# Kernel optimization log

Hardware: AMD Instinct MI355X
Metric: run time of the kernel (lower is better)

## Reference

```python
import jax, jax.numpy as jnp
import numpy as np

B, S, D, H = 4, 2048, 1024, 16
DEPTH = D // H
NEG = -1e9


def setup_inputs() -> dict:
    key = jax.random.key(0)
    ks = jax.random.split(key, 9)
    scale = 1.0 / np.sqrt(D)
    x = jax.random.normal(ks[0], (B, S, D), dtype=jnp.float32)
    # causal additive mask: 1 where future positions (masked), 0 elsewhere
    mask = jnp.triu(jnp.ones((S, S), dtype=jnp.float32), k=1)[None, None, :, :]
    wq = jax.random.normal(ks[1], (D, D), dtype=jnp.float32) * scale
    bq = jnp.zeros((D,), dtype=jnp.float32)
    wk = jax.random.normal(ks[2], (D, D), dtype=jnp.float32) * scale
    bk = jnp.zeros((D,), dtype=jnp.float32)
    wv = jax.random.normal(ks[3], (D, D), dtype=jnp.float32) * scale
    bv = jnp.zeros((D,), dtype=jnp.float32)
    wo = jax.random.normal(ks[4], (D, D), dtype=jnp.float32) * scale
    bo = jnp.zeros((D,), dtype=jnp.float32)
    return {"x": x, "mask": mask, "wq": wq, "bq": bq, "wk": wk, "bk": bk,
            "wv": wv, "bv": bv, "wo": wo, "bo": bo}


def _split_heads(t):
    # [B, S, D] -> [B, H, S, depth]
    return t.reshape(B, S, H, DEPTH).transpose(0, 2, 1, 3)


def reference(x, mask, wq, bq, wk, bk, wv, bv, wo, bo):
    q = _split_heads(x @ wq.T + bq)
    k = _split_heads(x @ wk.T + bk)
    v = _split_heads(x @ wv.T + bv)
    scores = jnp.einsum('bhqd,bhkd->bhqk', q, k) / jnp.sqrt(jnp.float32(DEPTH))
    scores = scores + mask * NEG
    attn = jax.nn.softmax(scores, axis=-1)
    out = jnp.einsum('bhqk,bhkd->bhqd', attn, v)  # [B, H, S, depth]
    out = out.transpose(0, 2, 1, 3).reshape(B, S, D)
    return out @ wo.T + bo
```

## Files before the change

### kernel.cpp

```cpp
#include <hip/hip_runtime.h>
#include <hip/hip_bf16.h>
#include <stdint.h>

typedef __attribute__((ext_vector_type(8))) short short8;
typedef __attribute__((ext_vector_type(4))) float f32x4;
typedef __attribute__((ext_vector_type(16))) float f32x16;

#define AS1 __attribute__((address_space(1)))
#define AS3 __attribute__((address_space(3)))

constexpr int Bc = 4, Sc = 2048, Dc = 1024, Hc = 16;

__device__ __forceinline__ unsigned short f2b(float x) {
  __hip_bfloat16 h = __float2bfloat16(x);
  return *reinterpret_cast<unsigned short*>(&h);
}

__device__ __forceinline__ uint32_t cvtpk(float lo, float hi) {
  uint32_t r;
  asm("v_cvt_pk_bf16_f32 %0, %1, %2" : "=v"(r) : "v"(lo), "v"(hi));
  return r;
}

__device__ __forceinline__ void glds16(const void* g, void* l) {
  __builtin_amdgcn_global_load_lds((const AS1 uint32_t*)g, (AS3 uint32_t*)l, 16, 0, 0);
}

__global__ void cast_f32_bf16_x4(const float* __restrict__ in,
                                 unsigned short* __restrict__ out, int n4) {
  int i = blockIdx.x * blockDim.x + threadIdx.x;
  if (i >= n4) return;
  float4 a = ((const float4*)in)[i];
  ushort4 o;
  o.x = f2b(a.x); o.y = f2b(a.y); o.z = f2b(a.z); o.w = f2b(a.w);
  ((ushort4*)out)[i] = o;
}

__global__ void cast_w4(const float* __restrict__ wq, const float* __restrict__ wk,
                        const float* __restrict__ wv, const float* __restrict__ wo,
                        unsigned short* __restrict__ oq, unsigned short* __restrict__ ok,
                        unsigned short* __restrict__ ov, unsigned short* __restrict__ oo) {
  int which = blockIdx.y;
  const float* in = which == 0 ? wq : which == 1 ? wk : which == 2 ? wv : wo;
  unsigned short* out = which == 0 ? oq : which == 1 ? ok : which == 2 ? ov : oo;
  int i = blockIdx.x * blockDim.x + threadIdx.x;
  float4 a = ((const float4*)in)[i];
  ushort4 o;
  o.x = f2b(a.x); o.y = f2b(a.y); o.z = f2b(a.z); o.w = f2b(a.w);
  ((ushort4*)out)[i] = o;
}

template<int MODE>
__device__ __forceinline__ void gemm128(
    const unsigned short* __restrict__ A, const unsigned short* __restrict__ W,
    const float* __restrict__ bias, void* __restrict__ outp,
    int m0, int n0, unsigned short (*lA)[128 * 32], unsigned short (*lB)[128 * 32])
{
  const int tid = threadIdx.x;
  const int w = tid >> 6, lane = tid & 63;
  const int g = lane >> 4, c = lane & 15;
  const int wr = w >> 1, wc = w & 1;

  f32x4 acc[4][4];
#pragma unroll
  for (int i = 0; i < 4; ++i)
#pragma unroll
    for (int j = 0; j < 4; ++j) acc[i][j] = f32x4{0.f, 0.f, 0.f, 0.f};

  const int srow = lane >> 2;
  const int gch = (lane & 3) ^ ((srow >> 1) & 3);
  const int rslot = (g ^ ((c >> 1) & 3)) * 16;

  auto stage = [&](int buf, int k0) {
#pragma unroll
    for (int i = 0; i < 2; ++i) {
      int row = i * 64 + w * 16 + srow;
      glds16(A + (size_t)(m0 + row) * 1024 + k0 + gch * 8,
             (char*)lA[buf] + i * 4096 + w * 1024);
      glds16(W + (size_t)(n0 + row) * 1024 + k0 + gch * 8,
             (char*)lB[buf] + i * 4096 + w * 1024);
    }
  };

  stage(0, 0);

  for (int t = 0; t < 32; ++t) {
    const int cur = t & 1;
    if (t + 1 < 32) {
      stage(cur ^ 1, (t + 1) * 32);
      asm volatile("s_waitcnt vmcnt(4)" ::: "memory");
    } else {
      asm volatile("s_waitcnt vmcnt(0)" ::: "memory");
    }
    __builtin_amdgcn_s_barrier();
    asm volatile("" ::: "memory");

    short8 aF[4], bF[4];
#pragma unroll
    for (int mt = 0; mt < 4; ++mt) {
      int row = wr * 64 + mt * 16 + c;
      aF[mt] = *(const short8*)((const char*)lA[cur] + row * 64 + rslot);
    }
#pragma unroll
    for (int nt = 0; nt < 4; ++nt) {
      int row = wc * 64 + nt * 16 + c;
      bF[nt] = *(const short8*)((const char*)lB[cur] + row * 64 + rslot);
    }
#pragma unroll
    for (int mt = 0; mt < 4; ++mt)
#pragma unroll
      for (int nt = 0; nt < 4; ++nt)
        acc[mt][nt] = __builtin_amdgcn_mfma_f32_16x16x32_bf16(aF[mt], bF[nt],
                                                              acc[mt][nt], 0, 0, 0);
    asm volatile("" ::: "memory");
    __builtin_amdgcn_s_barrier();
    asm volatile("" ::: "memory");
  }

#pragma unroll
  for (int mt = 0; mt < 4; ++mt) {
    int mg = m0 + wr * 64 + mt * 16 + 4 * g;
#pragma unroll
    for (int nt = 0; nt < 4; ++nt) {
      int ng = n0 + wc * 64 + nt * 16 + c;
      float bb_ = bias[ng];
      if constexpr (MODE == 0) {
        unsigned short* o = (unsigned short*)outp;
#pragma unroll
        for (int r = 0; r < 4; ++r)
          o[(size_t)(mg + r) * 1024 + ng] = f2b(acc[mt][nt][r] + bb_);
      } else if constexpr (MODE == 1) {
        unsigned short* o = (unsigned short*)outp;
        int bb = mg >> 11, s0 = mg & 2047;
        int hh = ng >> 6, dd = ng & 63;
        ushort4 pk;
        pk.x = f2b(acc[mt][nt][0] + bb_);
        pk.y = f2b(acc[mt][nt][1] + bb_);
        pk.z = f2b(acc[mt][nt][2] + bb_);
        pk.w = f2b(acc[mt][nt][3] + bb_);
        *(ushort4*)&o[(((size_t)bb * Hc + hh) * 64 + dd) * Sc + s0] = pk;
      } else {
        float* o = (float*)outp;
#pragma unroll
        for (int r = 0; r < 4; ++r)
          o[(size_t)(mg + r) * 1024 + ng] = acc[mt][nt][r] + bb_;
      }
    }
  }
}

__global__ __launch_bounds__(256) void qkv_gemm(
    const unsigned short* __restrict__ xb,
    const unsigned short* __restrict__ wqb, const unsigned short* __restrict__ wkb,
    const unsigned short* __restrict__ wvb,
    const float* __restrict__ bq, const float* __restrict__ bk,
    const float* __restrict__ bv,
    unsigned short* __restrict__ qo, unsigned short* __restrict__ ko,
    unsigned short* __restrict__ vto)
{
  __shared__ unsigned short lA[2][128 * 32], lB[2][128 * 32];
  int which = blockIdx.x >> 3;
  int n0 = (blockIdx.x & 7) * 128;
  int m0 = blockIdx.y * 128;
  if (which == 0)      gemm128<0>(xb, wqb, bq, qo, m0, n0, lA, lB);
  else if (which == 1) gemm128<0>(xb, wkb, bk, ko, m0, n0, lA, lB);
  else                 gemm128<1>(xb, wvb, bv, vto, m0, n0, lA, lB);
}

__global__ __launch_bounds__(256) void out_gemm(
    const unsigned short* __restrict__ ao, const unsigned short* __restrict__ wob,
    const float* __restrict__ bo, float* __restrict__ out)
{
  __shared__ unsigned short lA[2][128 * 32], lB[2][128 * 32];
  gemm128<2>(ao, wob, bo, out, blockIdx.y * 128, blockIdx.x * 128, lA, lB);
}

__global__ __launch_bounds__(256, 2) void attn_kernel(
    const unsigned short* __restrict__ qg, const unsigned short* __restrict__ kg,
    const unsigned short* __restrict__ vtg, unsigned short* __restrict__ ao)
{
  __shared__ unsigned short lK[2][64 * 64];
  __shared__ unsigned short lV[2][64 * 64];

  const int bh = blockIdx.x;
  const int qlo = blockIdx.y, qhi = 15 - qlo;
  const int b = bh >> 4, h = bh & 15;
  const int tid = threadIdx.x, w = tid >> 6, lane = tid & 63;
  const int qr = lane & 31, hi = lane >> 5;
  const int qb2[2] = { qlo * 128 + 32 * w, qhi * 128 + 32 * w };
  constexpr float CE = 0.125f * 1.44269504f;

  short8 qB[2][4];
#pragma unroll
  for (int qi = 0; qi < 2; ++qi) {
    const unsigned short* qp = qg + (size_t)(b * Sc + qb2[qi] + qr) * Dc + h * 64 + 8 * hi;
#pragma unroll
    for (int i = 0; i < 4; ++i)
      qB[qi][i] = *(const short8*)(qp + 16 * i);
  }

  float m_[2] = { -3e38f, -3e38f }, lv[2] = { 0.f, 0.f };
  f32x16 oT[2][2];
#pragma unroll
  for (int qi = 0; qi < 2; ++qi)
#pragma unroll
    for (int n = 0; n < 2; ++n)
#pragma unroll
      for (int r = 0; r < 16; ++r) oT[qi][n][r] = 0.f;

  const int srow8 = lane >> 3;
  const int sslot = lane & 7;
  const unsigned short* kb_ = kg + (size_t)b * Sc * Dc + h * 64;
  const unsigned short* vb_ = vtg + (size_t)bh * 64 * Sc;

  auto stage = [&](int buf, int t) {
    const int kv0 = t * 64;
#pragma unroll
    for (int i = 0; i < 2; ++i) {
      int row = i * 32 + w * 8 + srow8;
      int gch = sslot ^ (row & 7);
      glds16(kb_ + (size_t)(kv0 + row) * Dc + gch * 8,
             (char*)lK[buf] + i * 4096 + w * 1024);
      glds16(vb_ + (size_t)row * Sc + kv0 + gch * 8,
             (char*)lV[buf] + i * 4096 + w * 1024);
    }
  };

  const int ntl = 2 * (qhi + 1);
  stage(0, 0);
  asm volatile("s_waitcnt vmcnt(0)" ::: "memory");
  __builtin_amdgcn_s_barrier();
  asm volatile("" ::: "memory");

  for (int t = 0; t < ntl; ++t) {
    const int cur = t & 1;
    const int kv0 = t * 64;
    if (t + 1 < ntl) stage(cur ^ 1, t + 1);

    if (kv0 <= qb2[1] + 31) {
      short8 kA[2][4];
#pragma unroll
      for (int kblk = 0; kblk < 2; ++kblk) {
        const int row = kblk * 32 + qr;
        const int swz = (row & 7) << 4;
#pragma unroll
        for (int i = 0; i < 4; ++i)
          kA[kblk][i] = *(const short8*)((const char*)lK[cur] + row * 128 +
                          (((2 * i + hi) * 16) ^ swz));
      }

      short8 pB[2][4];
      bool act[2];
#pragma unroll
      for (int qi = 0; qi < 2; ++qi) {
        const int qbase = qb2[qi];
        act[qi] = (kv0 <= qbase + 31);
        if (!act[qi]) continue;

        f32x16 sT[2];
        __builtin_amdgcn_s_setprio(1);
#pragma unroll
        for (int kblk = 0; kblk < 2; ++kblk) {
          f32x16 s;
#pragma unroll
          for (int r = 0; r < 16; ++r) s[r] = 0.f;
#pragma unroll
          for (int i = 0; i < 4; ++i)
            s = __builtin_amdgcn_mfma_f32_32x32x16_bf16(kA[kblk][i], qB[qi][i],
                                                        s, 0, 0, 0);
          sT[kblk] = s;
        }
        __builtin_amdgcn_s_setprio(0);

        if (kv0 + 63 > qbase) {
          const int q = qbase + qr;
#pragma unroll
          for (int kblk = 0; kblk < 2; ++kblk)
#pragma unroll
            for (int r = 0; r < 16; ++r) {
              int k = kv0 + kblk * 32 + (r & 3) + 8 * (r >> 2) + 4 * hi;
              if (k > q) sT[kblk][r] = -1e30f;
            }
        }

        float mx = sT[0][0];
#pragma unroll
        for (int r = 1; r < 16; ++r) mx = fmaxf(mx, sT[0][r]);
#pragma unroll
        for (int r = 0; r < 16; ++r) mx = fmaxf(mx, sT[1][r]);
        mx = fmaxf(mx, __shfl_xor(mx, 32));

        if (!__all(mx <= m_[qi] + 64.f)) {
          const float mo = m_[qi];
          const float mn = fmaxf(mo, mx);
          const float sf = __builtin_amdgcn_exp2f((mo - mn) * CE);
          m_[qi] = mn;
          lv[qi] *= sf;
#pragma unroll
          for (int n = 0; n < 2; ++n)
#pragma unroll
            for (int r = 0; r < 16; ++r) oT[qi][n][r] *= sf;
        }
        const float mc = m_[qi] * CE;
        float ls = 0.f;
#pragma unroll
        for (int kblk = 0; kblk < 2; ++kblk)
#pragma unroll
          for (int r = 0; r < 16; ++r) {
            float p = __builtin_amdgcn_exp2f(sT[kblk][r] * CE - mc);
            sT[kblk][r] = p;
            ls += p;
          }
        lv[qi] += ls;

#pragma unroll
        for (int kblk = 0; kblk < 2; ++kblk) {
          uint32_t pk[4][2];
#pragma unroll
          for (int qp = 0; qp < 4; ++qp)
#pragma unroll
            for (int rp = 0; rp < 2; ++rp)
              pk[qp][rp] = cvtpk(sT[kblk][4 * qp + 2 * rp],
                                 sT[kblk][4 * qp + 2 * rp + 1]);
#pragma unroll
          for (int m2 = 0; m2 < 2; ++m2) {
            uint32_t s0 = hi ? pk[2 * m2][0] : pk[2 * m2 + 1][0];
            uint32_t s1 = hi ? pk[2 * m2][1] : pk[2 * m2 + 1][1];
            uint32_t r0 = __shfl_xor(s0, 32);
            uint32_t r1 = __shfl_xor(s1, 32);
            uint32_t w0 = hi ? r0 : pk[2 * m2][0];
            uint32_t w1 = hi ? r1 : pk[2 * m2][1];
            uint32_t w2 = hi ? pk[2 * m2 + 1][0] : r0;
            uint32_t w3 = hi ? pk[2 * m2 + 1][1] : r1;
            uint32_t tmp[4] = { w0, w1, w2, w3 };
            pB[qi][2 * kblk + m2] = *(const short8*)tmp;
          }
        }
      }

      short8 vA[2][4];
#pragma unroll
      for (int n = 0; n < 2; ++n) {
        const int row = 32 * n + qr;
        const int swz = (row & 7) << 4;
#pragma unroll
        for (int m = 0; m < 4; ++m)
          vA[n][m] = *(const short8*)((const char*)lV[cur] + row * 128 +
                       (((2 * m + hi) * 16) ^ swz));
      }

      __builtin_amdgcn_s_setprio(1);
#pragma unroll
      for (int qi = 0; qi < 2; ++qi) {
        if (!act[qi]) continue;
#pragma unroll
        for (int n = 0; n < 2; ++n)
#pragma unroll
          for (int m = 0; m < 4; ++m)
            oT[qi][n] = __builtin_amdgcn_mfma_f32_32x32x16_bf16(
                vA[n][m], pB[qi][m], oT[qi][n], 0, 0, 0);
      }
      __builtin_amdgcn_s_setprio(0);
    }

    asm volatile("s_waitcnt vmcnt(0)" ::: "memory");
    __builtin_amdgcn_s_barrier();
    asm volatile("" ::: "memory");
  }

#pragma unroll
  for (int qi = 0; qi < 2; ++qi) {
    float l = lv[qi] + __shfl_xor(lv[qi], 32);
    float inv = 1.0f / l;
    const int qrow = qb2[qi] + qr;
    unsigned short* op = ao + (size_t)(b * Sc + qrow) * Dc + h * 64;
#pragma unroll
    for (int n = 0; n < 2; ++n)
#pragma unroll
      for (int rg = 0; rg < 4; ++rg) {
        ushort4 pkv;
        pkv.x = f2b(oT[qi][n][4 * rg + 0] * inv);
        pkv.y = f2b(oT[qi][n][4 * rg + 1] * inv);
        pkv.z = f2b(oT[qi][n][4 * rg + 2] * inv);
        pkv.w = f2b(oT[qi][n][4 * rg + 3] * inv);
        *(ushort4*)(op + 32 * n + 8 * rg + 4 * hi) = pkv;
      }
  }
}

extern "C" void kernel_launch(void* const* d_in, const int* in_sizes, int n_in,
                              void* d_out, int out_size, void* d_ws, size_t ws_size,
                              hipStream_t stream) {
  const float* x  = (const float*)d_in[0];
  const float* wq = (const float*)d_in[2];
  const float* bq = (const float*)d_in[3];
  const float* wk = (const float*)d_in[4];
  const float* bk = (const float*)d_in[5];
  const float* wv = (const float*)d_in[6];
  const float* bv = (const float*)d_in[7];
  const float* wo = (const float*)d_in[8];
  const float* bo = (const float*)d_in[9];
  float* out = (float*)d_out;

  char* ws = (char*)d_ws;
  unsigned short* xb  = (unsigned short*)(ws);
  unsigned short* wqb = (unsigned short*)(ws + 16777216);
  unsigned short* wkb = (unsigned short*)(ws + 18874368);
  unsigned short* wvb = (unsigned short*)(ws + 20971520);
  unsigned short* wob = (unsigned short*)(ws + 23068672);
  unsigned short* qb  = (unsigned short*)(ws + 25165824);
  unsigned short* kb  = (unsigned short*)(ws + 41943040);
  unsigned short* vtb = (unsigned short*)(ws + 58720256);
  unsigned short* aob = (unsigned short*)(ws + 75497472);

  cast_f32_bf16_x4<<<8192, 256, 0, stream>>>(x, xb, 2097152);
  cast_w4<<<dim3(1024, 4), 256, 0, stream>>>(wq, wk, wv, wo, wqb, wkb, wvb, wob);

  qkv_gemm<<<dim3(24, 64), 256, 0, stream>>>(xb, wqb, wkb, wvb, bq, bk, bv,
                                             qb, kb, vtb);
  attn_kernel<<<dim3(64, 8), 256, 0, stream>>>(qb, kb, vtb, aob);
  out_gemm<<<dim3(8, 64), 256, 0, stream>>>(aob, wob, bo, out);
}
```

Baseline: 184.7 us.

## Use single-buffered BK=64 GEMM tiles with 8-way LDS swizzle and swap grid order

The shared GEMM routine moves from a double-buffered 32-wide K step (32 iterations, async prefetch overlapped with MFMA) to a single-buffered 64-wide K step (16 iterations), where the next tile is loaded only after compute and a barrier. The LDS layout uses an 8-slot XOR swizzle for 128-byte rows, and global pointers are precomputed and incremented. The grid is transposed so consecutive blocks walk along M instead of N, which changes L2 reuse of weight and activation tiles. Halving the barrier and iteration count trades against losing load/compute overlap within a block, leaning on occupancy to hide latency instead.

```diff
diff --git a/kernel.cpp b/kernel.cpp
--- a/kernel.cpp
+++ b/kernel.cpp
@@ -54,7 +54,7 @@
 __device__ __forceinline__ void gemm128(
     const unsigned short* __restrict__ A, const unsigned short* __restrict__ W,
     const float* __restrict__ bias, void* __restrict__ outp,
-    int m0, int n0, unsigned short (*lA)[128 * 32], unsigned short (*lB)[128 * 32])
+    int m0, int n0, unsigned short* lA, unsigned short* lB)
 {
   const int tid = threadIdx.x;
   const int w = tid >> 6, lane = tid & 63;
@@ -67,55 +67,63 @@
 #pragma unroll
     for (int j = 0; j < 4; ++j) acc[i][j] = f32x4{0.f, 0.f, 0.f, 0.f};
 
-  const int srow = lane >> 2;
-  const int gch = (lane & 3) ^ ((srow >> 1) & 3);
-  const int rslot = (g ^ ((c >> 1) & 3)) * 16;
-
-  auto stage = [&](int buf, int k0) {
-#pragma unroll
-    for (int i = 0; i < 2; ++i) {
-      int row = i * 64 + w * 16 + srow;
-      glds16(A + (size_t)(m0 + row) * 1024 + k0 + gch * 8,
-             (char*)lA[buf] + i * 4096 + w * 1024);
-      glds16(W + (size_t)(n0 + row) * 1024 + k0 + gch * 8,
-             (char*)lB[buf] + i * 4096 + w * 1024);
-    }
-  };
-
-  stage(0, 0);
-
-  for (int t = 0; t < 32; ++t) {
-    const int cur = t & 1;
-    if (t + 1 < 32) {
-      stage(cur ^ 1, (t + 1) * 32);
-      asm volatile("s_waitcnt vmcnt(4)" ::: "memory");
-    } else {
-      asm volatile("s_waitcnt vmcnt(0)" ::: "memory");
-    }
+  const int lrow8 = lane >> 3;
+  const int gslot = (lane & 7) ^ lrow8;
+
+  const unsigned short* ap[4];
+  const unsigned short* bp[4];
+#pragma unroll
+  for (int j = 0; j < 4; ++j) {
+    int row = (j * 4 + w) * 8 + lrow8;
+    ap[j] = A + (size_t)(m0 + row) * 1024 + gslot * 8;
+    bp[j] = W + (size_t)(n0 + row) * 1024 + gslot * 8;
+  }
+
+  const int sl0 = (g ^ (c & 7)) << 4;
+  const int sl1 = ((4 ^ g) ^ (c & 7)) << 4;
+  const char* lA0 = (const char*)lA + (wr * 64 + c) * 128 + sl0;
+  const char* lA1 = (const char*)lA + (wr * 64 + c) * 128 + sl1;
+  const char* lB0 = (const char*)lB + (wc * 64 + c) * 128 + sl0;
+  const char* lB1 = (const char*)lB + (wc * 64 + c) * 128 + sl1;
+
+#define STAGE                                               \
+  do {                                                      \
+    _Pragma("unroll")                                       \
+    for (int j = 0; j < 4; ++j) {                           \
+      glds16(ap[j], (char*)lA + (j * 4 + w) * 1024);        \
+      glds16(bp[j], (char*)lB + (j * 4 + w) * 1024);        \
+      ap[j] += 64; bp[j] += 64;                             \
+    }                                                       \
+  } while (0)
+
+  STAGE;
+  for (int t = 0; t < 16; ++t) {
+    asm volatile("s_waitcnt vmcnt(0)" ::: "memory");
     __builtin_amdgcn_s_barrier();
     asm volatile("" ::: "memory");
 
-    short8 aF[4], bF[4];
-#pragma unroll
-    for (int mt = 0; mt < 4; ++mt) {
-      int row = wr * 64 + mt * 16 + c;
-      aF[mt] = *(const short8*)((const char*)lA[cur] + row * 64 + rslot);
+#pragma unroll
+    for (int ks = 0; ks < 2; ++ks) {
+      short8 aF[4], bF[4];
+#pragma unroll
+      for (int mt = 0; mt < 4; ++mt)
+        aF[mt] = *(const short8*)((ks ? lA1 : lA0) + mt * 2048);
+#pragma unroll
+      for (int nt = 0; nt < 4; ++nt)
+        bF[nt] = *(const short8*)((ks ? lB1 : lB0) + nt * 2048);
+#pragma unroll
+      for (int mt = 0; mt < 4; ++mt)
+#pragma unroll
+        for (int nt = 0; nt < 4; ++nt)
+          acc[mt][nt] = __builtin_amdgcn_mfma_f32_16x16x32_bf16(
+              aF[mt], bF[nt], acc[mt][nt], 0, 0, 0);
     }
-#pragma unroll
-    for (int nt = 0; nt < 4; ++nt) {
-      int row = wc * 64 + nt * 16 + c;
-      bF[nt] = *(const short8*)((const char*)lB[cur] + row * 64 + rslot);
-    }
-#pragma unroll
-    for (int mt = 0; mt < 4; ++mt)
-#pragma unroll
-      for (int nt = 0; nt < 4; ++nt)
-        acc[mt][nt] = __builtin_amdgcn_mfma_f32_16x16x32_bf16(aF[mt], bF[nt],
-                                                              acc[mt][nt], 0, 0, 0);
     asm volatile("" ::: "memory");
     __builtin_amdgcn_s_barrier();
     asm volatile("" ::: "memory");
-  }
+    if (t + 1 < 16) STAGE;
+  }
+#undef STAGE
 
 #pragma unroll
   for (int mt = 0; mt < 4; ++mt) {
@@ -158,10 +166,10 @@
     unsigned short* __restrict__ qo, unsigned short* __restrict__ ko,
     unsigned short* __restrict__ vto)
 {
-  __shared__ unsigned short lA[2][128 * 32], lB[2][128 * 32];
-  int which = blockIdx.x >> 3;
-  int n0 = (blockIdx.x & 7) * 128;
-  int m0 = blockIdx.y * 128;
+  __shared__ unsigned short lA[128 * 64], lB[128 * 64];
+  int m0 = blockIdx.x * 128;
+  int which = blockIdx.y >> 3;
+  int n0 = (blockIdx.y & 7) * 128;
   if (which == 0)      gemm128<0>(xb, wqb, bq, qo, m0, n0, lA, lB);
   else if (which == 1) gemm128<0>(xb, wkb, bk, ko, m0, n0, lA, lB);
   else                 gemm128<1>(xb, wvb, bv, vto, m0, n0, lA, lB);
@@ -171,8 +179,8 @@
     const unsigned short* __restrict__ ao, const unsigned short* __restrict__ wob,
     const float* __restrict__ bo, float* __restrict__ out)
 {
-  __shared__ unsigned short lA[2][128 * 32], lB[2][128 * 32];
-  gemm128<2>(ao, wob, bo, out, blockIdx.y * 128, blockIdx.x * 128, lA, lB);
+  __shared__ unsigned short lA[128 * 64], lB[128 * 64];
+  gemm128<2>(ao, wob, bo, out, blockIdx.x * 128, blockIdx.y * 128, lA, lB);
 }
 
 __global__ __launch_bounds__(256, 2) void attn_kernel(
@@ -416,8 +424,8 @@
   cast_f32_bf16_x4<<<8192, 256, 0, stream>>>(x, xb, 2097152);
   cast_w4<<<dim3(1024, 4), 256, 0, stream>>>(wq, wk, wv, wo, wqb, wkb, wvb, wob);
 
-  qkv_gemm<<<dim3(24, 64), 256, 0, stream>>>(xb, wqb, wkb, wvb, bq, bk, bv,
+  qkv_gemm<<<dim3(64, 24), 256, 0, stream>>>(xb, wqb, wkb, wvb, bq, bk, bv,
                                              qb, kb, vtb);
   attn_kernel<<<dim3(64, 8), 256, 0, stream>>>(qb, kb, vtb, aob);
-  out_gemm<<<dim3(8, 64), 256, 0, stream>>>(aob, wob, bo, out);
-}
+  out_gemm<<<dim3(64, 8), 256, 0, stream>>>(aob, wob, bo, out);
+}
```

New measurement: 161.4 us. 12.6% less time.
